# Kernel optimization log

Measured on AMD Instinct MI355X. Metric: run time of the kernel, lower is better.

## Reference

```python
import jax, jax.numpy as jnp
import numpy as np

HIDDEN, FFN, N_EXPERTS, TOP_K = 1024, 2816, 8, 2


def setup_inputs() -> dict:
    key = jax.random.key(0)
    k1, k2, k3, k4, k5 = jax.random.split(key, 5)
    hidden_states = jax.random.normal(k1, (1, 2048, HIDDEN), dtype=jnp.float32)
    # torch Linear weights: [out, in]; experts stacked on leading E axis
    Wgate = jax.random.normal(k2, (N_EXPERTS, HIDDEN), dtype=jnp.float32) * 0.02
    Wg = jax.random.normal(k3, (N_EXPERTS, FFN, HIDDEN), dtype=jnp.float32) * 0.02
    Wu = jax.random.normal(k4, (N_EXPERTS, FFN, HIDDEN), dtype=jnp.float32) * 0.02
    Wd = jax.random.normal(k5, (N_EXPERTS, HIDDEN, FFN), dtype=jnp.float32) * 0.02
    return {"hidden_states": hidden_states, "Wgate": Wgate, "Wg": Wg, "Wu": Wu, "Wd": Wd}


def reference(hidden_states, Wgate, Wg, Wu, Wd):
    x = hidden_states.reshape(-1, hidden_states.shape[-1])  # [T, H]
    # --- router ---
    logits = jnp.einsum('th,eh->te', x, Wgate)               # [T, E]
    weights = jax.nn.softmax(logits, axis=-1)
    topk_w, topk_i = jax.lax.top_k(weights, TOP_K)           # [T, K]
    topk_w = topk_w / jnp.sum(topk_w, axis=-1, keepdims=True)
    # per-token per-expert combine weight (zero if expert not in top-k)
    comb = jnp.sum(jax.nn.one_hot(topk_i, N_EXPERTS, dtype=x.dtype) * topk_w[..., None], axis=1)  # [T, E]
    # --- all-expert SwiGLU (dense reference for the gather-compute-scatter loop) ---
    g = jnp.einsum('th,efh->tef', x, Wg)                     # [T, E, F]
    u = jnp.einsum('th,efh->tef', x, Wu)
    h = jax.nn.silu(g) * u
    y = jnp.einsum('tef,ehf->teh', h, Wd)                    # [T, E, H]
    out = jnp.einsum('te,teh->th', comb, y)                  # [T, H]
    return out
```

## Files before the change

kernel.cpp:

```cpp
#include <hip/hip_runtime.h>
#include <hip/hip_bf16.h>

#define HIDDEN 1024
#define FFN    2816
#define NEXP   8
#define NTOK   2048

typedef __attribute__((ext_vector_type(8))) short short8;
typedef __attribute__((ext_vector_type(4))) short bf16x4;
typedef __attribute__((ext_vector_type(4))) float f32x4;

static __device__ __forceinline__ short f2bf(float f) {
    __hip_bfloat16 h = __float2bfloat16(f);
    return *(short*)&h;
}

static __device__ __forceinline__ void gl_lds16(const short* g, short* l) {
    __builtin_amdgcn_global_load_lds(
        (const __attribute__((address_space(1))) void*)g,
        (__attribute__((address_space(3))) void*)l, 16, 0, 0);
}

#define WAITV(N) asm volatile("s_waitcnt vmcnt(" #N ")" ::: "memory")
#define LGKM0    asm volatile("s_waitcnt lgkmcnt(0)" ::: "memory")
#define BAR()    do { __builtin_amdgcn_s_barrier(); \
                      __builtin_amdgcn_sched_barrier(0); } while (0)

static __device__ __forceinline__ void
router_body(int t, int lane, const float* __restrict__ x,
            const float* __restrict__ Wgate, int* __restrict__ counts,
            int* __restrict__ tok, float* __restrict__ wts)
{
    float acc[NEXP];
#pragma unroll
    for (int e = 0; e < NEXP; e++) acc[e] = 0.f;
    const float* xrow = x + (size_t)t * HIDDEN;
    for (int h = lane; h < HIDDEN; h += 64) {
        float xv = xrow[h];
#pragma unroll
        for (int e = 0; e < NEXP; e++) acc[e] += xv * Wgate[e * HIDDEN + h];
    }
#pragma unroll
    for (int off = 32; off > 0; off >>= 1) {
#pragma unroll
        for (int e = 0; e < NEXP; e++) acc[e] += __shfl_down(acc[e], off);
    }
    if (lane == 0) {
        float mx = acc[0];
#pragma unroll
        for (int e = 1; e < NEXP; e++) mx = fmaxf(mx, acc[e]);
        float p[NEXP];
#pragma unroll
        for (int e = 0; e < NEXP; e++) p[e] = __expf(acc[e] - mx);
        int i0 = 0; float p0 = p[0];
#pragma unroll
        for (int e = 1; e < NEXP; e++) if (p[e] > p0) { p0 = p[e]; i0 = e; }
        int i1 = -1; float p1 = -1.f;
#pragma unroll
        for (int e = 0; e < NEXP; e++) {
            if (e == i0) continue;
            if (p[e] > p1) { p1 = p[e]; i1 = e; }
        }
        float inv = 1.f / (p0 + p1);
        float w0 = p0 * inv, w1 = p1 * inv;
        int s0 = atomicAdd(&counts[i0], 1);
        tok[i0 * NTOK + s0] = t; wts[i0 * NTOK + s0] = w0;
        int s1 = atomicAdd(&counts[i1], 1);
        tok[i1 * NTOK + s1] = t; wts[i1 * NTOK + s1] = w1;
    }
}

__global__ void __launch_bounds__(64)
router_kernel(const float* __restrict__ x, const float* __restrict__ Wgate,
              int* __restrict__ counts, int* __restrict__ tok,
              float* __restrict__ wts)
{
    router_body(blockIdx.x, threadIdx.x, x, Wgate, counts, tok, wts);
}

__global__ void __launch_bounds__(256)
fused_rxz(const float* __restrict__ x, const float* __restrict__ Wgate,
          int* __restrict__ counts, int* __restrict__ tok,
          float* __restrict__ wts, short* __restrict__ xbf,
          float* __restrict__ out)
{
    int bid = blockIdx.x;
    int tid = threadIdx.x;
    if (bid < 512) {
        router_body(bid * 4 + (tid >> 6), tid & 63, x, Wgate, counts, tok, wts);
        return;
    }
    if (bid < 1024) {
        long long base4 = (long long)(bid - 512) * 1024;
#pragma unroll
        for (int p = 0; p < 4; p++) {
            long long r = base4 + p * 256 + tid;
            float4 a = ((const float4*)x)[r];
            bf16x4 o;
            o[0] = f2bf(a.x); o[1] = f2bf(a.y); o[2] = f2bf(a.z); o[3] = f2bf(a.w);
            *(bf16x4*)(xbf + 4 * r) = o;
        }
        return;
    }
    long long base4 = (long long)(bid - 1024) * 1024;
    float4 z = make_float4(0.f, 0.f, 0.f, 0.f);
#pragma unroll
    for (int p = 0; p < 4; p++)
        ((float4*)out)[base4 + p * 256 + tid] = z;
}

#define FFN1_BLOCKS 2816
__global__ void __launch_bounds__(256, 2)
ffn1_v10(const short* __restrict__ xbf, const float* __restrict__ Wg,
         const float* __restrict__ Wu, const int* __restrict__ counts,
         const int* __restrict__ tok, short* __restrict__ hbuf)
{
    int bid = blockIdx.x;
    int tid = threadIdx.x;
    int xb  = bid / 176;
    int yz  = bid - xb * 176;
    int e   = yz / 22;
    int fb  = yz - e * 22;
    int cnt = counts[e];
    int row0 = xb * 128;
    if (row0 >= cnt) return;
    int off_e = 0;
#pragma unroll
    for (int i = 0; i < NEXP; i++) if (i < e) off_e += counts[i];
    int f0 = fb * 128;

    __shared__ short Xs[2][128 * 32];
    __shared__ short Gs[2][128 * 32];
    __shared__ short Us[2][128 * 32];
    __shared__ int   stok[128];

    if (tid < 128) stok[tid] = tok[e * NTOK + min(row0 + tid, cnt - 1)];
    __syncthreads();

    int lane = tid & 63, w = tid >> 6;
    int l15 = lane & 15, lq = lane >> 4;
    int wm = (w & 1) * 64, wn = (w >> 1) * 64;

    int prow   = lane >> 2;
    int gchunk = (lane & 3) ^ ((lane >> 3) & 3);
    const short* xsrc[2]; const float* gsrc[2]; const float* usrc[2];
    int rb[2];
#pragma unroll
    for (int j = 0; j < 2; j++) {
        int rbase = w * 32 + j * 16;
        int r = rbase + prow;
        xsrc[j] = xbf + (size_t)stok[r] * HIDDEN + gchunk * 8;
        gsrc[j] = Wg + (size_t)e * FFN * HIDDEN + (size_t)(f0 + r) * HIDDEN + gchunk * 8;
        usrc[j] = Wu + (size_t)e * FFN * HIDDEN + (size_t)(f0 + r) * HIDDEN + gchunk * 8;
        rb[j] = rbase * 32;
    }
    int wadr0 = rb[0] + lane * 8;
    int wadr1 = rb[1] + lane * 8;

    int aoff[4], boff[4];
#pragma unroll
    for (int mi = 0; mi < 4; mi++) {
        int r = wm + mi * 16 + l15;
        aoff[mi] = r * 32 + (lq ^ ((r >> 1) & 3)) * 8;
    }
#pragma unroll
    for (int ni = 0; ni < 4; ni++) {
        int r = wn + ni * 16 + l15;
        boff[ni] = r * 32 + (lq ^ ((r >> 1) & 3)) * 8;
    }

    f32x4 cg[4][4], cu[4][4];
#pragma unroll
    for (int i = 0; i < 4; i++)
#pragma unroll
        for (int j = 0; j < 4; j++) { cg[i][j] = (f32x4)0.f; cu[i][j] = (f32x4)0.f; }

    float4 g0a, g0b, g1a, g1b, u0a, u0b, u1a, u1b;

#define XDMA(B, T) do { int _k = (T) * 32;                          \
    gl_lds16(xsrc[0] + _k, &Xs[B][rb[0]]);                          \
    gl_lds16(xsrc[1] + _k, &Xs[B][rb[1]]); } while (0)

#define LOADR(T) do { int _k = (T) * 32;                            \
    g0a = *(const float4*)(gsrc[0] + _k);                           \
    g0b = *(const float4*)(gsrc[0] + _k + 4);                       \
    g1a = *(const float4*)(gsrc[1] + _k);                           \
    g1b = *(const float4*)(gsrc[1] + _k + 4);                       \
    u0a = *(const float4*)(usrc[0] + _k);                           \
    u0b = *(const float4*)(usrc[0] + _k + 4);                       \
    u1a = *(const float4*)(usrc[1] + _k);                           \
    u1b = *(const float4*)(usrc[1] + _k + 4); } while (0)

#define PK8(dst, A, Bv) do { short8 _o;                             \
    _o[0] = f2bf(A.x);  _o[1] = f2bf(A.y);                          \
    _o[2] = f2bf(A.z);  _o[3] = f2bf(A.w);                          \
    _o[4] = f2bf(Bv.x); _o[5] = f2bf(Bv.y);                         \
    _o[6] = f2bf(Bv.z); _o[7] = f2bf(Bv.w);                         \
    *(short8*)(dst) = _o; } while (0)

#define CVTW(B) do {                                                \
    PK8(&Gs[B][wadr0], g0a, g0b); PK8(&Gs[B][wadr1], g1a, g1b);     \
    PK8(&Us[B][wadr0], u0a, u0b); PK8(&Us[B][wadr1], u1a, u1b); } while (0)

#define COMP1(B) do {                                               \
    short8 af[4];                                                   \
    _Pragma("unroll")                                               \
    for (int mi = 0; mi < 4; mi++)                                  \
        af[mi] = *(const short8*)&Xs[B][aoff[mi]];                  \
    {   short8 bb[4];                                               \
        _Pragma("unroll")                                           \
        for (int ni = 0; ni < 4; ni++)                              \
            bb[ni] = *(const short8*)&Gs[B][boff[ni]];              \
        _Pragma("unroll")                                           \
        for (int mi = 0; mi < 4; mi++)                              \
        _Pragma("unroll")                                           \
        for (int ni = 0; ni < 4; ni++)                              \
            cg[mi][ni] = __builtin_amdgcn_mfma_f32_16x16x32_bf16(af[mi], bb[ni], cg[mi][ni], 0, 0, 0); \
    }                                                               \
    {   short8 bb[4];                                               \
        _Pragma("unroll")                                           \
        for (int ni = 0; ni < 4; ni++)                              \
            bb[ni] = *(const short8*)&Us[B][boff[ni]];              \
        _Pragma("unroll")                                           \
        for (int mi = 0; mi < 4; mi++)                              \
        _Pragma("unroll")                                           \
        for (int ni = 0; ni < 4; ni++)                              \
            cu[mi][ni] = __builtin_amdgcn_mfma_f32_16x16x32_bf16(af[mi], bb[ni], cu[mi][ni], 0, 0, 0); \
    } } while (0)

    XDMA(0, 0); LOADR(0);

    for (int tt = 0; tt < 32; tt += 2) {
        CVTW(0);
        XDMA(1, tt + 1); LOADR(tt + 1);
        WAITV(10); LGKM0; BAR();
        COMP1(0);
        BAR();
        CVTW(1);
        if (tt + 2 < 32) { XDMA(0, tt + 2); LOADR(tt + 2); WAITV(10); }
        else             { WAITV(0); }
        LGKM0; BAR();
        COMP1(1);
        BAR();
    }

#undef XDMA
#undef LOADR
#undef CVTW
#undef COMP1

#pragma unroll
    for (int mi = 0; mi < 4; mi++)
#pragma unroll
        for (int r = 0; r < 4; r++) {
            int row = wm + mi * 16 + lq * 4 + r;
            int grow = row0 + row;
            if (grow < cnt) {
                short* hrow = hbuf + (size_t)(off_e + grow) * FFN + f0 + wn;
#pragma unroll
                for (int ni = 0; ni < 4; ni++) {
                    float g = cg[mi][ni][r], u = cu[mi][ni][r];
                    float h = g / (1.f + __expf(-g)) * u;
                    hrow[ni * 16 + l15] = f2bf(h);
                }
            }
        }
}

__global__ void __launch_bounds__(256, 2)
ffn2_v9(const short* __restrict__ hbuf, const float* __restrict__ Wd,
        const int* __restrict__ counts, const int* __restrict__ tok,
        const float* __restrict__ wts, float* __restrict__ out)
{
    int bid = blockIdx.x;
    int xb  = bid >> 7;
    int yz  = bid & 127;
    int e   = yz >> 4;
    int y   = yz & 15;
    int cnt = counts[e];
    int row0 = xb * 128;
    if (row0 >= cnt) return;
    int off_e = 0;
#pragma unroll
    for (int i = 0; i < NEXP; i++) if (i < e) off_e += counts[i];
    int h0    = (y >> 1) * 128;
    int kbase = (y & 1) * (FFN / 2);

    __shared__ short Hs[2][128 * 32];
    __shared__ short Ds[2][128 * 32];
    __shared__ int   stok[128];
    __shared__ float swt[128];

    int tid = threadIdx.x;
    if (tid < 128) {
        int rc = min(row0 + tid, cnt - 1);
        stok[tid] = tok[e * NTOK + rc];
        swt[tid]  = wts[e * NTOK + rc];
    }
    __syncthreads();

    int lane = tid & 63, w = tid >> 6;
    int l15 = lane & 15, lq = lane >> 4;
    int wm = (w & 1) * 64, wn = (w >> 1) * 64;

    int prow   = lane >> 2;
    int gchunk = (lane & 3) ^ ((lane >> 3) & 3);
    const short* hsrc[2]; const float* dsrc[2];
    int rb[2];
#pragma unroll
    for (int j = 0; j < 2; j++) {
        int rbase = w * 32 + j * 16;
        int r = rbase + prow;
        hsrc[j] = hbuf + (size_t)(off_e + min(row0 + r, cnt - 1)) * FFN + kbase + gchunk * 8;
        dsrc[j] = Wd + (size_t)e * HIDDEN * FFN + (size_t)(h0 + r) * FFN + kbase + gchunk * 8;
        rb[j] = rbase * 32;
    }
    int wadr0 = rb[0] + lane * 8;
    int wadr1 = rb[1] + lane * 8;

    int aoff[4], boff[4];
#pragma unroll
    for (int mi = 0; mi < 4; mi++) {
        int r = wm + mi * 16 + l15;
        aoff[mi] = r * 32 + (lq ^ ((r >> 1) & 3)) * 8;
    }
#pragma unroll
    for (int ni = 0; ni < 4; ni++) {
        int r = wn + ni * 16 + l15;
        boff[ni] = r * 32 + (lq ^ ((r >> 1) & 3)) * 8;
    }

    f32x4 c[4][4];
#pragma unroll
    for (int i = 0; i < 4; i++)
#pragma unroll
        for (int j = 0; j < 4; j++) c[i][j] = (f32x4)0.f;

    float4 d0a, d0b, d1a, d1b;

#define HDMA(B, T) do { int _k = (T) * 32;                          \
    gl_lds16(hsrc[0] + _k, &Hs[B][rb[0]]);                          \
    gl_lds16(hsrc[1] + _k, &Hs[B][rb[1]]); } while (0)

#define LOADD(T) do { int _k = (T) * 32;                            \
    d0a = *(const float4*)(dsrc[0] + _k);                           \
    d0b = *(const float4*)(dsrc[0] + _k + 4);                       \
    d1a = *(const float4*)(dsrc[1] + _k);                           \
    d1b = *(const float4*)(dsrc[1] + _k + 4); } while (0)

#define CVTD(B) do {                                                \
    PK8(&Ds[B][wadr0], d0a, d0b); PK8(&Ds[B][wadr1], d1a, d1b); } while (0)

#define COMP2(B) do {                                               \
    short8 af[4], bd[4];                                            \
    _Pragma("unroll")                                               \
    for (int mi = 0; mi < 4; mi++)                                  \
        af[mi] = *(const short8*)&Hs[B][aoff[mi]];                  \
    _Pragma("unroll")                                               \
    for (int ni = 0; ni < 4; ni++)                                  \
        bd[ni] = *(const short8*)&Ds[B][boff[ni]];                  \
    _Pragma("unroll")                                               \
    for (int mi = 0; mi < 4; mi++)                                  \
    _Pragma("unroll")                                               \
    for (int ni = 0; ni < 4; ni++)                                  \
        c[mi][ni] = __builtin_amdgcn_mfma_f32_16x16x32_bf16(af[mi], bd[ni], c[mi][ni], 0, 0, 0); \
    } while (0)

    HDMA(0, 0); LOADD(0);

    for (int tt = 0; tt < 44; tt += 2) {
        CVTD(0);
        HDMA(1, tt + 1); LOADD(tt + 1);
        WAITV(6); LGKM0; BAR();
        COMP2(0);
        BAR();
        CVTD(1);
        if (tt + 2 < 44) { HDMA(0, tt + 2); LOADD(tt + 2); WAITV(6); }
        else             { WAITV(0); }
        LGKM0; BAR();
        COMP2(1);
        BAR();
    }

#undef HDMA
#undef LOADD
#undef CVTD
#undef COMP2
#undef PK8

#pragma unroll
    for (int mi = 0; mi < 4; mi++)
#pragma unroll
        for (int r = 0; r < 4; r++) {
            int row = wm + mi * 16 + lq * 4 + r;
            int grow = row0 + row;
            if (grow < cnt) {
                int t = stok[row];
                float wgt = swt[row];
                float* orow = out + (size_t)t * HIDDEN + h0 + wn;
#pragma unroll
                for (int ni = 0; ni < 4; ni++)
                    atomicAdd(&orow[ni * 16 + l15], wgt * c[mi][ni][r]);
            }
        }
}

#define LDW 40
__global__ void __launch_bounds__(256, 2)
ffn1_fb(const float* __restrict__ x, const float* __restrict__ Wg,
        const float* __restrict__ Wu, const int* __restrict__ counts,
        const int* __restrict__ tok, __hip_bfloat16* __restrict__ hbuf)
{
    int e = blockIdx.z;
    int cnt = counts[e];
    int row0 = blockIdx.x * 128;
    if (row0 >= cnt) return;
    int off_e = 0;
#pragma unroll
    for (int i = 0; i < NEXP; i++) if (i < e) off_e += counts[i];
    int f0 = blockIdx.y * 64;

    __shared__ short Xs[128][LDW];
    __shared__ short Gs[64][LDW];
    __shared__ short Us[64][LDW];
    __shared__ int   stok[128];

    int tid = threadIdx.x;
    if (tid < 128) stok[tid] = tok[e * NTOK + min(row0 + tid, cnt - 1)];
    __syncthreads();

    int lane = tid & 63, w = tid >> 6;
    int wm = (w & 1) * 64, wn = (w >> 1) * 32;
    int l15 = lane & 15, lq = lane >> 4;

    f32x4 cg[4][2], cu[4][2];
#pragma unroll
    for (int i = 0; i < 4; i++)
#pragma unroll
        for (int j = 0; j < 2; j++) { cg[i][j] = (f32x4)0.f; cu[i][j] = (f32x4)0.f; }

    const float* Wge = Wg + (size_t)e * FFN * HIDDEN;
    const float* Wue = Wu + (size_t)e * FFN * HIDDEN;

    int xr[4], xc[4]; const float* xp[4];
#pragma unroll
    for (int i = 0; i < 4; i++) {
        int idx = tid + 256 * i;
        xr[i] = idx >> 3; xc[i] = (idx & 7) * 4;
        xp[i] = x + (size_t)stok[xr[i]] * HIDDEN + xc[i];
    }
    int wr[2], wc[2]; const float* gp[2]; const float* up[2];
#pragma unroll
    for (int i = 0; i < 2; i++) {
        int idx = tid + 256 * i;
        wr[i] = idx >> 3; wc[i] = (idx & 7) * 4;
        gp[i] = Wge + (size_t)(f0 + wr[i]) * HIDDEN + wc[i];
        up[i] = Wue + (size_t)(f0 + wr[i]) * HIDDEN + wc[i];
    }

    float4 xa[4], ga[2], ua[2];
#pragma unroll
    for (int i = 0; i < 4; i++) xa[i] = *(const float4*)(xp[i]);
#pragma unroll
    for (int i = 0; i < 2; i++) { ga[i] = *(const float4*)(gp[i]); ua[i] = *(const float4*)(up[i]); }

    for (int k0 = 0; k0 < HIDDEN; k0 += 32) {
        __syncthreads();
#pragma unroll
        for (int i = 0; i < 4; i++) {
            short* d = &Xs[xr[i]][xc[i]];
            d[0] = f2bf(xa[i].x); d[1] = f2bf(xa[i].y);
            d[2] = f2bf(xa[i].z); d[3] = f2bf(xa[i].w);
        }
#pragma unroll
        for (int i = 0; i < 2; i++) {
            short* d = &Gs[wr[i]][wc[i]];
            d[0] = f2bf(ga[i].x); d[1] = f2bf(ga[i].y);
            d[2] = f2bf(ga[i].z); d[3] = f2bf(ga[i].w);
            short* d2 = &Us[wr[i]][wc[i]];
            d2[0] = f2bf(ua[i].x); d2[1] = f2bf(ua[i].y);
            d2[2] = f2bf(ua[i].z); d2[3] = f2bf(ua[i].w);
        }
        __syncthreads();
        if (k0 + 32 < HIDDEN) {
            int kn = k0 + 32;
#pragma unroll
            for (int i = 0; i < 4; i++) xa[i] = *(const float4*)(xp[i] + kn);
#pragma unroll
            for (int i = 0; i < 2; i++) { ga[i] = *(const float4*)(gp[i] + kn); ua[i] = *(const float4*)(up[i] + kn); }
        }
        short8 af[4], bg[2], bu[2];
#pragma unroll
        for (int mi = 0; mi < 4; mi++) af[mi] = *(const short8*)&Xs[wm + mi * 16 + l15][lq * 8];
#pragma unroll
        for (int ni = 0; ni < 2; ni++) {
            bg[ni] = *(const short8*)&Gs[wn + ni * 16 + l15][lq * 8];
            bu[ni] = *(const short8*)&Us[wn + ni * 16 + l15][lq * 8];
        }
#pragma unroll
        for (int mi = 0; mi < 4; mi++)
#pragma unroll
            for (int ni = 0; ni < 2; ni++) {
                cg[mi][ni] = __builtin_amdgcn_mfma_f32_16x16x32_bf16(af[mi], bg[ni], cg[mi][ni], 0, 0, 0);
                cu[mi][ni] = __builtin_amdgcn_mfma_f32_16x16x32_bf16(af[mi], bu[ni], cu[mi][ni], 0, 0, 0);
            }
    }

#pragma unroll
    for (int mi = 0; mi < 4; mi++)
#pragma unroll
        for (int r = 0; r < 4; r++) {
            int row = wm + mi * 16 + lq * 4 + r;
            int grow = row0 + row;
            if (grow < cnt) {
                __hip_bfloat16* hrow = hbuf + (size_t)(off_e + grow) * FFN + f0 + wn;
#pragma unroll
                for (int ni = 0; ni < 2; ni++) {
                    float g = cg[mi][ni][r], u = cu[mi][ni][r];
                    float h = g / (1.f + __expf(-g)) * u;
                    hrow[ni * 16 + l15] = __float2bfloat16(h);
                }
            }
        }
}

__global__ void __launch_bounds__(256, 2)
ffn2_fb(const __hip_bfloat16* __restrict__ hbuf, const float* __restrict__ Wd,
        const int* __restrict__ counts, const int* __restrict__ tok,
        const float* __restrict__ wts, float* __restrict__ out)
{
    int e = blockIdx.z;
    int cnt = counts[e];
    int row0 = blockIdx.x * 128;
    if (row0 >= cnt) return;
    int off_e = 0;
#pragma unroll
    for (int i = 0; i < NEXP; i++) if (i < e) off_e += counts[i];
    int h0 = blockIdx.y * 64;

    __shared__ short Hs[128][LDW];
    __shared__ short Ds[64][LDW];
    __shared__ int   stok[128];
    __shared__ float swt[128];

    int tid = threadIdx.x;
    if (tid < 128) {
        int rc = min(row0 + tid, cnt - 1);
        stok[tid] = tok[e * NTOK + rc];
        swt[tid]  = wts[e * NTOK + rc];
    }
    __syncthreads();

    int lane = tid & 63, w = tid >> 6;
    int wm = (w & 1) * 64, wn = (w >> 1) * 32;
    int l15 = lane & 15, lq = lane >> 4;

    f32x4 c[4][2];
#pragma unroll
    for (int i = 0; i < 4; i++)
#pragma unroll
        for (int j = 0; j < 2; j++) c[i][j] = (f32x4)0.f;

    const float* Wde = Wd + (size_t)e * HIDDEN * FFN;

    int hr[2], hc[2]; const short* hp[2];
#pragma unroll
    for (int i = 0; i < 2; i++) {
        int idx = tid + 256 * i;
        hr[i] = idx >> 2; hc[i] = (idx & 3) * 8;
        int ar = min(row0 + hr[i], cnt - 1);
        hp[i] = (const short*)(hbuf + (size_t)(off_e + ar) * FFN + hc[i]);
    }
    int dr[2], dc[2]; const float* dp[2];
#pragma unroll
    for (int i = 0; i < 2; i++) {
        int idx = tid + 256 * i;
        dr[i] = idx >> 3; dc[i] = (idx & 7) * 4;
        dp[i] = Wde + (size_t)(h0 + dr[i]) * FFN + dc[i];
    }

    short8 ha[2]; float4 da[2];
#pragma unroll
    for (int i = 0; i < 2; i++) { ha[i] = *(const short8*)(hp[i]); da[i] = *(const float4*)(dp[i]); }

    for (int k0 = 0; k0 < FFN; k0 += 32) {
        __syncthreads();
#pragma unroll
        for (int i = 0; i < 2; i++) {
            *(short8*)&Hs[hr[i]][hc[i]] = ha[i];
            short* d = &Ds[dr[i]][dc[i]];
            d[0] = f2bf(da[i].x); d[1] = f2bf(da[i].y);
            d[2] = f2bf(da[i].z); d[3] = f2bf(da[i].w);
        }
        __syncthreads();
        if (k0 + 32 < FFN) {
            int kn = k0 + 32;
#pragma unroll
            for (int i = 0; i < 2; i++) { ha[i] = *(const short8*)(hp[i] + kn); da[i] = *(const float4*)(dp[i] + kn); }
        }
        short8 af[4], bf_[2];
#pragma unroll
        for (int mi = 0; mi < 4; mi++) af[mi] = *(const short8*)&Hs[wm + mi * 16 + l15][lq * 8];
#pragma unroll
        for (int ni = 0; ni < 2; ni++) bf_[ni] = *(const short8*)&Ds[wn + ni * 16 + l15][lq * 8];
#pragma unroll
        for (int mi = 0; mi < 4; mi++)
#pragma unroll
            for (int ni = 0; ni < 2; ni++)
                c[mi][ni] = __builtin_amdgcn_mfma_f32_16x16x32_bf16(af[mi], bf_[ni], c[mi][ni], 0, 0, 0);
    }

#pragma unroll
    for (int mi = 0; mi < 4; mi++)
#pragma unroll
        for (int r = 0; r < 4; r++) {
            int row = wm + mi * 16 + lq * 4 + r;
            int grow = row0 + row;
            if (grow < cnt) {
                int t = stok[row];
                float wgt = swt[row];
                float* orow = out + (size_t)t * HIDDEN + h0 + wn;
#pragma unroll
                for (int ni = 0; ni < 2; ni++)
                    atomicAdd(&orow[ni * 16 + l15], wgt * c[mi][ni][r]);
            }
        }
}

extern "C" void kernel_launch(void* const* d_in, const int* in_sizes, int n_in,
                              void* d_out, int out_size, void* d_ws, size_t ws_size,
                              hipStream_t stream) {
    const float* x     = (const float*)d_in[0];
    const float* Wgate = (const float*)d_in[1];
    const float* Wg    = (const float*)d_in[2];
    const float* Wu    = (const float*)d_in[3];
    const float* Wd    = (const float*)d_in[4];
    float* out = (float*)d_out;

    char* ws = (char*)d_ws;
    int*   counts = (int*)ws;
    int*   tok    = (int*)(ws + 256);
    float* wts    = (float*)(ws + 256 + NEXP * NTOK * 4);

    hipMemsetAsync(counts, 0, 256, stream);

    const size_t base = 256 + 2 * (size_t)NEXP * NTOK * 4;
    const size_t NEED = base
        + 2ull * NTOK * HIDDEN
        + 2ull * 2ull * NTOK * FFN;

    if (ws_size >= NEED) {
        short* xbf  = (short*)(ws + base);
        short* hbuf = xbf + (size_t)NTOK * HIDDEN;

        fused_rxz<<<1536, 256, 0, stream>>>(x, Wgate, counts, tok, wts, xbf, out);

        ffn1_v10<<<FFN1_BLOCKS, 256, 0, stream>>>(xbf, Wg, Wu, counts, tok, hbuf);

        ffn2_v9<<<2048, 256, 0, stream>>>(hbuf, Wd, counts, tok, wts, out);
    } else {
        hipMemsetAsync(out, 0, (size_t)out_size * sizeof(float), stream);
        router_kernel<<<NTOK, 64, 0, stream>>>(x, Wgate, counts, tok, wts);
        __hip_bfloat16* hbuf = (__hip_bfloat16*)(ws + base);
        dim3 g1(NTOK / 128, FFN / 64, NEXP);
        ffn1_fb<<<g1, 256, 0, stream>>>(x, Wg, Wu, counts, tok, hbuf);
        dim3 g2(NTOK / 128, HIDDEN / 64, NEXP);
        ffn2_fb<<<g2, 256, 0, stream>>>(hbuf, Wd, counts, tok, wts, out);
    }
}
```

Baseline: 447.0 us.

## Use 512-thread FFN blocks, read fp32 x directly, fold output zeroing into FFN1

Both FFN kernels move from 256 to 512 threads per block, so each wave owns a 64x32 sub-tile instead of 64x64 and stages one 16-row slice per operand. FFN1 now loads fp32 x rows and converts them to bf16 itself, which removes the separate x-to-bf16 conversion pass and its workspace buffer. Zeroing the output moves into extra blocks of the FFN1 launch, and the router runs as its own small kernel. The cost is that the gathered x rows are read and converted again by every FFN1 block that uses them, and FFN1 loses its async LDS DMA for X in favour of register loads and conversion.

```diff
diff --git a/kernel.cpp b/kernel.cpp
--- a/kernel.cpp
+++ b/kernel.cpp
@@ -13,6 +13,13 @@
 static __device__ __forceinline__ short f2bf(float f) {
     __hip_bfloat16 h = __float2bfloat16(f);
     return *(short*)&h;
+}
+
+static __device__ __forceinline__ void pk8(short* dst, float4 A, float4 B) {
+    short8 o;
+    o[0] = f2bf(A.x); o[1] = f2bf(A.y); o[2] = f2bf(A.z); o[3] = f2bf(A.w);
+    o[4] = f2bf(B.x); o[5] = f2bf(B.y); o[6] = f2bf(B.z); o[7] = f2bf(B.w);
+    *(short8*)dst = o;
 }
 
 static __device__ __forceinline__ void gl_lds16(const short* g, short* l) {
@@ -79,44 +86,31 @@
 }
 
 __global__ void __launch_bounds__(256)
-fused_rxz(const float* __restrict__ x, const float* __restrict__ Wgate,
-          int* __restrict__ counts, int* __restrict__ tok,
-          float* __restrict__ wts, short* __restrict__ xbf,
-          float* __restrict__ out)
+router4(const float* __restrict__ x, const float* __restrict__ Wgate,
+        int* __restrict__ counts, int* __restrict__ tok,
+        float* __restrict__ wts)
+{
+    router_body(blockIdx.x * 4 + (threadIdx.x >> 6), threadIdx.x & 63,
+                x, Wgate, counts, tok, wts);
+}
+
+#define FFN1_BLOCKS 2816
+#define ZERO_BLOCKS 256
+__global__ void __launch_bounds__(512, 2)
+ffn1_v11(const float* __restrict__ x, const float* __restrict__ Wg,
+         const float* __restrict__ Wu, const int* __restrict__ counts,
+         const int* __restrict__ tok, short* __restrict__ hbuf,
+         float* __restrict__ out)
 {
     int bid = blockIdx.x;
     int tid = threadIdx.x;
-    if (bid < 512) {
-        router_body(bid * 4 + (tid >> 6), tid & 63, x, Wgate, counts, tok, wts);
+    if (bid >= FFN1_BLOCKS) {
+        long long b4 = (long long)(bid - FFN1_BLOCKS) * 2048 + tid;
+        float4 z = make_float4(0.f, 0.f, 0.f, 0.f);
+#pragma unroll
+        for (int p = 0; p < 4; p++) ((float4*)out)[b4 + p * 512] = z;
         return;
     }
-    if (bid < 1024) {
-        long long base4 = (long long)(bid - 512) * 1024;
-#pragma unroll
-        for (int p = 0; p < 4; p++) {
-            long long r = base4 + p * 256 + tid;
-            float4 a = ((const float4*)x)[r];
-            bf16x4 o;
-            o[0] = f2bf(a.x); o[1] = f2bf(a.y); o[2] = f2bf(a.z); o[3] = f2bf(a.w);
-            *(bf16x4*)(xbf + 4 * r) = o;
-        }
-        return;
-    }
-    long long base4 = (long long)(bid - 1024) * 1024;
-    float4 z = make_float4(0.f, 0.f, 0.f, 0.f);
-#pragma unroll
-    for (int p = 0; p < 4; p++)
-        ((float4*)out)[base4 + p * 256 + tid] = z;
-}
-
-#define FFN1_BLOCKS 2816
-__global__ void __launch_bounds__(256, 2)
-ffn1_v10(const short* __restrict__ xbf, const float* __restrict__ Wg,
-         const float* __restrict__ Wu, const int* __restrict__ counts,
-         const int* __restrict__ tok, short* __restrict__ hbuf)
-{
-    int bid = blockIdx.x;
-    int tid = threadIdx.x;
     int xb  = bid / 176;
     int yz  = bid - xb * 176;
     int e   = yz / 22;
@@ -132,121 +126,87 @@
     __shared__ short Xs[2][128 * 32];
     __shared__ short Gs[2][128 * 32];
     __shared__ short Us[2][128 * 32];
-    __shared__ int   stok[128];
-
-    if (tid < 128) stok[tid] = tok[e * NTOK + min(row0 + tid, cnt - 1)];
-    __syncthreads();
 
     int lane = tid & 63, w = tid >> 6;
     int l15 = lane & 15, lq = lane >> 4;
-    int wm = (w & 1) * 64, wn = (w >> 1) * 64;
+    int wm = (w & 1) * 64, wn = (w >> 1) * 32;
 
     int prow   = lane >> 2;
     int gchunk = (lane & 3) ^ ((lane >> 3) & 3);
-    const short* xsrc[2]; const float* gsrc[2]; const float* usrc[2];
-    int rb[2];
-#pragma unroll
-    for (int j = 0; j < 2; j++) {
-        int rbase = w * 32 + j * 16;
-        int r = rbase + prow;
-        xsrc[j] = xbf + (size_t)stok[r] * HIDDEN + gchunk * 8;
-        gsrc[j] = Wg + (size_t)e * FFN * HIDDEN + (size_t)(f0 + r) * HIDDEN + gchunk * 8;
-        usrc[j] = Wu + (size_t)e * FFN * HIDDEN + (size_t)(f0 + r) * HIDDEN + gchunk * 8;
-        rb[j] = rbase * 32;
-    }
-    int wadr0 = rb[0] + lane * 8;
-    int wadr1 = rb[1] + lane * 8;
-
-    int aoff[4], boff[4];
+    int rbase  = w * 16;
+    int srow   = min(row0 + rbase + prow, cnt - 1);
+    int tkn    = tok[e * NTOK + srow];
+    const float* xsrc = x  + (size_t)tkn * HIDDEN + gchunk * 8;
+    const float* gsrc = Wg + (size_t)e * FFN * HIDDEN
+                           + (size_t)(f0 + rbase + prow) * HIDDEN + gchunk * 8;
+    const float* usrc = Wu + (size_t)e * FFN * HIDDEN
+                           + (size_t)(f0 + rbase + prow) * HIDDEN + gchunk * 8;
+    int wadr = rbase * 32 + lane * 8;
+
+    int aoff[4], boff[2];
 #pragma unroll
     for (int mi = 0; mi < 4; mi++) {
         int r = wm + mi * 16 + l15;
         aoff[mi] = r * 32 + (lq ^ ((r >> 1) & 3)) * 8;
     }
 #pragma unroll
-    for (int ni = 0; ni < 4; ni++) {
+    for (int ni = 0; ni < 2; ni++) {
         int r = wn + ni * 16 + l15;
         boff[ni] = r * 32 + (lq ^ ((r >> 1) & 3)) * 8;
     }
 
-    f32x4 cg[4][4], cu[4][4];
+    f32x4 cg[4][2], cu[4][2];
 #pragma unroll
     for (int i = 0; i < 4; i++)
 #pragma unroll
-        for (int j = 0; j < 4; j++) { cg[i][j] = (f32x4)0.f; cu[i][j] = (f32x4)0.f; }
-
-    float4 g0a, g0b, g1a, g1b, u0a, u0b, u1a, u1b;
-
-#define XDMA(B, T) do { int _k = (T) * 32;                          \
-    gl_lds16(xsrc[0] + _k, &Xs[B][rb[0]]);                          \
-    gl_lds16(xsrc[1] + _k, &Xs[B][rb[1]]); } while (0)
-
-#define LOADR(T) do { int _k = (T) * 32;                            \
-    g0a = *(const float4*)(gsrc[0] + _k);                           \
-    g0b = *(const float4*)(gsrc[0] + _k + 4);                       \
-    g1a = *(const float4*)(gsrc[1] + _k);                           \
-    g1b = *(const float4*)(gsrc[1] + _k + 4);                       \
-    u0a = *(const float4*)(usrc[0] + _k);                           \
-    u0b = *(const float4*)(usrc[0] + _k + 4);                       \
-    u1a = *(const float4*)(usrc[1] + _k);                           \
-    u1b = *(const float4*)(usrc[1] + _k + 4); } while (0)
-
-#define PK8(dst, A, Bv) do { short8 _o;                             \
-    _o[0] = f2bf(A.x);  _o[1] = f2bf(A.y);                          \
-    _o[2] = f2bf(A.z);  _o[3] = f2bf(A.w);                          \
-    _o[4] = f2bf(Bv.x); _o[5] = f2bf(Bv.y);                         \
-    _o[6] = f2bf(Bv.z); _o[7] = f2bf(Bv.w);                         \
-    *(short8*)(dst) = _o; } while (0)
-
-#define CVTW(B) do {                                                \
-    PK8(&Gs[B][wadr0], g0a, g0b); PK8(&Gs[B][wadr1], g1a, g1b);     \
-    PK8(&Us[B][wadr0], u0a, u0b); PK8(&Us[B][wadr1], u1a, u1b); } while (0)
+        for (int j = 0; j < 2; j++) { cg[i][j] = (f32x4)0.f; cu[i][j] = (f32x4)0.f; }
+
+    float4 xa_, xb_, ga_, gb_, ua_, ub_;
+
+#define LOAD1(T) do { int _k = (T) * 32;                            \
+    xa_ = *(const float4*)(xsrc + _k); xb_ = *(const float4*)(xsrc + _k + 4); \
+    ga_ = *(const float4*)(gsrc + _k); gb_ = *(const float4*)(gsrc + _k + 4); \
+    ua_ = *(const float4*)(usrc + _k); ub_ = *(const float4*)(usrc + _k + 4); } while (0)
+
+#define CVT1(B) do {                                                \
+    pk8(&Xs[B][wadr], xa_, xb_);                                    \
+    pk8(&Gs[B][wadr], ga_, gb_);                                    \
+    pk8(&Us[B][wadr], ua_, ub_); } while (0)
 
 #define COMP1(B) do {                                               \
-    short8 af[4];                                                   \
+    short8 af[4], bg[2], bu[2];                                     \
     _Pragma("unroll")                                               \
     for (int mi = 0; mi < 4; mi++)                                  \
         af[mi] = *(const short8*)&Xs[B][aoff[mi]];                  \
-    {   short8 bb[4];                                               \
-        _Pragma("unroll")                                           \
-        for (int ni = 0; ni < 4; ni++)                              \
-            bb[ni] = *(const short8*)&Gs[B][boff[ni]];              \
-        _Pragma("unroll")                                           \
-        for (int mi = 0; mi < 4; mi++)                              \
-        _Pragma("unroll")                                           \
-        for (int ni = 0; ni < 4; ni++)                              \
-            cg[mi][ni] = __builtin_amdgcn_mfma_f32_16x16x32_bf16(af[mi], bb[ni], cg[mi][ni], 0, 0, 0); \
+    _Pragma("unroll")                                               \
+    for (int ni = 0; ni < 2; ni++) {                                \
+        bg[ni] = *(const short8*)&Gs[B][boff[ni]];                  \
+        bu[ni] = *(const short8*)&Us[B][boff[ni]];                  \
     }                                                               \
-    {   short8 bb[4];                                               \
-        _Pragma("unroll")                                           \
-        for (int ni = 0; ni < 4; ni++)                              \
-            bb[ni] = *(const short8*)&Us[B][boff[ni]];              \
-        _Pragma("unroll")                                           \
-        for (int mi = 0; mi < 4; mi++)                              \
-        _Pragma("unroll")                                           \
-        for (int ni = 0; ni < 4; ni++)                              \
-            cu[mi][ni] = __builtin_amdgcn_mfma_f32_16x16x32_bf16(af[mi], bb[ni], cu[mi][ni], 0, 0, 0); \
+    _Pragma("unroll")                                               \
+    for (int mi = 0; mi < 4; mi++)                                  \
+    _Pragma("unroll")                                               \
+    for (int ni = 0; ni < 2; ni++) {                                \
+        cg[mi][ni] = __builtin_amdgcn_mfma_f32_16x16x32_bf16(af[mi], bg[ni], cg[mi][ni], 0, 0, 0); \
+        cu[mi][ni] = __builtin_amdgcn_mfma_f32_16x16x32_bf16(af[mi], bu[ni], cu[mi][ni], 0, 0, 0); \
     } } while (0)
 
-    XDMA(0, 0); LOADR(0);
-
+    LOAD1(0);
     for (int tt = 0; tt < 32; tt += 2) {
-        CVTW(0);
-        XDMA(1, tt + 1); LOADR(tt + 1);
-        WAITV(10); LGKM0; BAR();
+        CVT1(0);
+        LOAD1(tt + 1);
+        LGKM0; BAR();
         COMP1(0);
         BAR();
-        CVTW(1);
-        if (tt + 2 < 32) { XDMA(0, tt + 2); LOADR(tt + 2); WAITV(10); }
-        else             { WAITV(0); }
+        CVT1(1);
+        if (tt + 2 < 32) LOAD1(tt + 2);
         LGKM0; BAR();
         COMP1(1);
         BAR();
     }
 
-#undef XDMA
-#undef LOADR
-#undef CVTW
+#undef LOAD1
+#undef CVT1
 #undef COMP1
 
 #pragma unroll
@@ -258,7 +218,7 @@
             if (grow < cnt) {
                 short* hrow = hbuf + (size_t)(off_e + grow) * FFN + f0 + wn;
 #pragma unroll
-                for (int ni = 0; ni < 4; ni++) {
+                for (int ni = 0; ni < 2; ni++) {
                     float g = cg[mi][ni][r], u = cu[mi][ni][r];
                     float h = g / (1.f + __expf(-g)) * u;
                     hrow[ni * 16 + l15] = f2bf(h);
@@ -267,10 +227,10 @@
         }
 }
 
-__global__ void __launch_bounds__(256, 2)
-ffn2_v9(const short* __restrict__ hbuf, const float* __restrict__ Wd,
-        const int* __restrict__ counts, const int* __restrict__ tok,
-        const float* __restrict__ wts, float* __restrict__ out)
+__global__ void __launch_bounds__(512, 2)
+ffn2_v11(const short* __restrict__ hbuf, const float* __restrict__ Wd,
+         const int* __restrict__ counts, const int* __restrict__ tok,
+         const float* __restrict__ wts, float* __restrict__ out)
 {
     int bid = blockIdx.x;
     int xb  = bid >> 7;
@@ -301,81 +261,68 @@
 
     int lane = tid & 63, w = tid >> 6;
     int l15 = lane & 15, lq = lane >> 4;
-    int wm = (w & 1) * 64, wn = (w >> 1) * 64;
+    int wm = (w & 1) * 64, wn = (w >> 1) * 32;
 
     int prow   = lane >> 2;
     int gchunk = (lane & 3) ^ ((lane >> 3) & 3);
-    const short* hsrc[2]; const float* dsrc[2];
-    int rb[2];
-#pragma unroll
-    for (int j = 0; j < 2; j++) {
-        int rbase = w * 32 + j * 16;
-        int r = rbase + prow;
-        hsrc[j] = hbuf + (size_t)(off_e + min(row0 + r, cnt - 1)) * FFN + kbase + gchunk * 8;
-        dsrc[j] = Wd + (size_t)e * HIDDEN * FFN + (size_t)(h0 + r) * FFN + kbase + gchunk * 8;
-        rb[j] = rbase * 32;
-    }
-    int wadr0 = rb[0] + lane * 8;
-    int wadr1 = rb[1] + lane * 8;
-
-    int aoff[4], boff[4];
+    int rbase  = w * 16;
+    const short* hsrc = hbuf + (size_t)(off_e + min(row0 + rbase + prow, cnt - 1)) * FFN
+                             + kbase + gchunk * 8;
+    const float* dsrc = Wd + (size_t)e * HIDDEN * FFN
+                           + (size_t)(h0 + rbase + prow) * FFN + kbase + gchunk * 8;
+    int wadr = rbase * 32 + lane * 8;
+
+    int aoff[4], boff[2];
 #pragma unroll
     for (int mi = 0; mi < 4; mi++) {
         int r = wm + mi * 16 + l15;
         aoff[mi] = r * 32 + (lq ^ ((r >> 1) & 3)) * 8;
     }
 #pragma unroll
-    for (int ni = 0; ni < 4; ni++) {
+    for (int ni = 0; ni < 2; ni++) {
         int r = wn + ni * 16 + l15;
         boff[ni] = r * 32 + (lq ^ ((r >> 1) & 3)) * 8;
     }
 
-    f32x4 c[4][4];
+    f32x4 c[4][2];
 #pragma unroll
     for (int i = 0; i < 4; i++)
 #pragma unroll
-        for (int j = 0; j < 4; j++) c[i][j] = (f32x4)0.f;
-
-    float4 d0a, d0b, d1a, d1b;
-
-#define HDMA(B, T) do { int _k = (T) * 32;                          \
-    gl_lds16(hsrc[0] + _k, &Hs[B][rb[0]]);                          \
-    gl_lds16(hsrc[1] + _k, &Hs[B][rb[1]]); } while (0)
+        for (int j = 0; j < 2; j++) c[i][j] = (f32x4)0.f;
+
+    float4 da_, db_;
+
+#define HDMA(B, T) gl_lds16(hsrc + (T) * 32, &Hs[B][rbase * 32])
 
 #define LOADD(T) do { int _k = (T) * 32;                            \
-    d0a = *(const float4*)(dsrc[0] + _k);                           \
-    d0b = *(const float4*)(dsrc[0] + _k + 4);                       \
-    d1a = *(const float4*)(dsrc[1] + _k);                           \
-    d1b = *(const float4*)(dsrc[1] + _k + 4); } while (0)
-
-#define CVTD(B) do {                                                \
-    PK8(&Ds[B][wadr0], d0a, d0b); PK8(&Ds[B][wadr1], d1a, d1b); } while (0)
+    da_ = *(const float4*)(dsrc + _k);                              \
+    db_ = *(const float4*)(dsrc + _k + 4); } while (0)
 
 #define COMP2(B) do {                                               \
-    short8 af[4], bd[4];                                            \
+    short8 af[4], bd[2];                                            \
     _Pragma("unroll")                                               \
     for (int mi = 0; mi < 4; mi++)                                  \
         af[mi] = *(const short8*)&Hs[B][aoff[mi]];                  \
     _Pragma("unroll")                                               \
-    for (int ni = 0; ni < 4; ni++)                                  \
+    for (int ni = 0; ni < 2; ni++)                                  \
         bd[ni] = *(const short8*)&Ds[B][boff[ni]];                  \
     _Pragma("unroll")                                               \
     for (int mi = 0; mi < 4; mi++)                                  \
     _Pragma("unroll")                                               \
-    for (int ni = 0; ni < 4; ni++)                                  \
+    for (int ni = 0; ni < 2; ni++)                                  \
         c[mi][ni] = __builtin_amdgcn_mfma_f32_16x16x32_bf16(af[mi], bd[ni], c[mi][ni], 0, 0, 0); \
     } while (0)
 
     HDMA(0, 0); LOADD(0);
 
     for (int tt = 0; tt < 44; tt += 2) {
-        CVTD(0);
+        pk8(&Ds[0][wadr], da_, db_);
         HDMA(1, tt + 1); LOADD(tt + 1);
-        WAITV(6); LGKM0; BAR();
+        WAITV(3); LGKM0; BAR();
         COMP2(0);
         BAR();
-        CVTD(1);
-        if (tt + 2 < 44) { HDMA(0, tt + 2); LOADD(tt + 2); WAITV(6); }
+        pk8(&Ds[1][wadr], da_, db_);
+        if (tt + 2 < 44) { HDMA(0, tt + 2); LOADD(tt + 2); WAITV(3); }
         else             { WAITV(0); }
         LGKM0; BAR();
         COMP2(1);
@@ -384,9 +331,7 @@
 
 #undef HDMA
 #undef LOADD
-#undef CVTD
 #undef COMP2
-#undef PK8
 
 #pragma unroll
     for (int mi = 0; mi < 4; mi++)
@@ -399,7 +344,7 @@
                 float wgt = swt[row];
                 float* orow = out + (size_t)t * HIDDEN + h0 + wn;
 #pragma unroll
-                for (int ni = 0; ni < 4; ni++)
+                for (int ni = 0; ni < 2; ni++)
                     atomicAdd(&orow[ni * 16 + l15], wgt * c[mi][ni][r]);
             }
         }
@@ -645,19 +590,17 @@
     hipMemsetAsync(counts, 0, 256, stream);
 
     const size_t base = 256 + 2 * (size_t)NEXP * NTOK * 4;
-    const size_t NEED = base
-        + 2ull * NTOK * HIDDEN
-        + 2ull * 2ull * NTOK * FFN;
+    const size_t NEED = base + 2ull * 2ull * NTOK * FFN;
 
     if (ws_size >= NEED) {
-        short* xbf  = (short*)(ws + base);
-        short* hbuf = xbf + (size_t)NTOK * HIDDEN;
-
-        fused_rxz<<<1536, 256, 0, stream>>>(x, Wgate, counts, tok, wts, xbf, out);
-
-        ffn1_v10<<<FFN1_BLOCKS, 256, 0, stream>>>(xbf, Wg, Wu, counts, tok, hbuf);
-
-        ffn2_v9<<<2048, 256, 0, stream>>>(hbuf, Wd, counts, tok, wts, out);
+        short* hbuf = (short*)(ws + base);
+
+        router4<<<512, 256, 0, stream>>>(x, Wgate, counts, tok, wts);
+
+        ffn1_v11<<<FFN1_BLOCKS + ZERO_BLOCKS, 512, 0, stream>>>(
+            x, Wg, Wu, counts, tok, hbuf, out);
+
+        ffn2_v11<<<2048, 512, 0, stream>>>(hbuf, Wd, counts, tok, wts, out);
     } else {
         hipMemsetAsync(out, 0, (size_t)out_size * sizeof(float), stream);
         router_kernel<<<NTOK, 64, 0, stream>>>(x, Wgate, counts, tok, wts);
```

Result: slower. 482.0 us (+7.8%).

## Double token tile to 256 rows with 512-thread blocks in both FFN kernels

Applied to the files above, without the earlier changes.

Both expert GEMM kernels now process 256 gathered tokens per block using eight waves instead of 128 tokens with four waves. Each wave loads one 16-row slice of the fp32 weight tile rather than two, and the launch grids are halved. The goal is to halve how many times each expert's fp32 weights are read from memory and converted to bf16, since that weight traffic dominates. The costs are more LDS per block, higher register pressure at 512 threads, and more wasted padded rows for experts whose token count is not a multiple of 256.

```diff
diff --git a/kernel.cpp b/kernel.cpp
--- a/kernel.cpp
+++ b/kernel.cpp
@@ -13,6 +13,13 @@
 static __device__ __forceinline__ short f2bf(float f) {
     __hip_bfloat16 h = __float2bfloat16(f);
     return *(short*)&h;
+}
+
+static __device__ __forceinline__ void pk8(short* dst, float4 A, float4 B) {
+    short8 o;
+    o[0] = f2bf(A.x); o[1] = f2bf(A.y); o[2] = f2bf(A.z); o[3] = f2bf(A.w);
+    o[4] = f2bf(B.x); o[5] = f2bf(B.y); o[6] = f2bf(B.z); o[7] = f2bf(B.w);
+    *(short8*)dst = o;
 }
 
 static __device__ __forceinline__ void gl_lds16(const short* g, short* l) {
@@ -109,9 +116,9 @@
         ((float4*)out)[base4 + p * 256 + tid] = z;
 }
 
-#define FFN1_BLOCKS 2816
-__global__ void __launch_bounds__(256, 2)
-ffn1_v10(const short* __restrict__ xbf, const float* __restrict__ Wg,
+#define FFN1_BLOCKS 1408
+__global__ void __launch_bounds__(512, 2)
+ffn1_v12(const short* __restrict__ xbf, const float* __restrict__ Wg,
          const float* __restrict__ Wu, const int* __restrict__ counts,
          const int* __restrict__ tok, short* __restrict__ hbuf)
 {
@@ -122,40 +129,40 @@
     int e   = yz / 22;
     int fb  = yz - e * 22;
     int cnt = counts[e];
-    int row0 = xb * 128;
+    int row0 = xb * 256;
     if (row0 >= cnt) return;
     int off_e = 0;
 #pragma unroll
     for (int i = 0; i < NEXP; i++) if (i < e) off_e += counts[i];
     int f0 = fb * 128;
 
-    __shared__ short Xs[2][128 * 32];
+    __shared__ short Xs[2][256 * 32];
     __shared__ short Gs[2][128 * 32];
     __shared__ short Us[2][128 * 32];
-    __shared__ int   stok[128];
-
-    if (tid < 128) stok[tid] = tok[e * NTOK + min(row0 + tid, cnt - 1)];
+    __shared__ int   stok[256];
+
+    if (tid < 256) stok[tid] = tok[e * NTOK + min(row0 + tid, cnt - 1)];
     __syncthreads();
 
     int lane = tid & 63, w = tid >> 6;
     int l15 = lane & 15, lq = lane >> 4;
-    int wm = (w & 1) * 64, wn = (w >> 1) * 64;
+    int wm = (w & 3) * 64, wn = (w >> 2) * 64;
 
     int prow   = lane >> 2;
     int gchunk = (lane & 3) ^ ((lane >> 3) & 3);
-    const short* xsrc[2]; const float* gsrc[2]; const float* usrc[2];
-    int rb[2];
+
+    const short* xsrc[2]; int xrb[2];
 #pragma unroll
     for (int j = 0; j < 2; j++) {
         int rbase = w * 32 + j * 16;
-        int r = rbase + prow;
-        xsrc[j] = xbf + (size_t)stok[r] * HIDDEN + gchunk * 8;
-        gsrc[j] = Wg + (size_t)e * FFN * HIDDEN + (size_t)(f0 + r) * HIDDEN + gchunk * 8;
-        usrc[j] = Wu + (size_t)e * FFN * HIDDEN + (size_t)(f0 + r) * HIDDEN + gchunk * 8;
-        rb[j] = rbase * 32;
-    }
-    int wadr0 = rb[0] + lane * 8;
-    int wadr1 = rb[1] + lane * 8;
+        xsrc[j] = xbf + (size_t)stok[rbase + prow] * HIDDEN + gchunk * 8;
+        xrb[j] = rbase * 32;
+    }
+    const float* gsrc = Wg + (size_t)e * FFN * HIDDEN
+                           + (size_t)(f0 + w * 16 + prow) * HIDDEN + gchunk * 8;
+    const float* usrc = Wu + (size_t)e * FFN * HIDDEN
+                           + (size_t)(f0 + w * 16 + prow) * HIDDEN + gchunk * 8;
+    int wadr = (w * 16) * 32 + lane * 8;
 
     int aoff[4], boff[4];
 #pragma unroll
@@ -175,32 +182,19 @@
 #pragma unroll
         for (int j = 0; j < 4; j++) { cg[i][j] = (f32x4)0.f; cu[i][j] = (f32x4)0.f; }
 
-    float4 g0a, g0b, g1a, g1b, u0a, u0b, u1a, u1b;
+    float4 ga_, gb_, ua_, ub_;
 
 #define XDMA(B, T) do { int _k = (T) * 32;                          \
-    gl_lds16(xsrc[0] + _k, &Xs[B][rb[0]]);                          \
-    gl_lds16(xsrc[1] + _k, &Xs[B][rb[1]]); } while (0)
+    gl_lds16(xsrc[0] + _k, &Xs[B][xrb[0]]);                         \
+    gl_lds16(xsrc[1] + _k, &Xs[B][xrb[1]]); } while (0)
 
 #define LOADR(T) do { int _k = (T) * 32;                            \
-    g0a = *(const float4*)(gsrc[0] + _k);                           \
-    g0b = *(const float4*)(gsrc[0] + _k + 4);                       \
-    g1a = *(const float4*)(gsrc[1] + _k);                           \
-    g1b = *(const float4*)(gsrc[1] + _k + 4);                       \
-    u0a = *(const float4*)(usrc[0] + _k);                           \
-    u0b = *(const float4*)(usrc[0] + _k + 4);                       \
-    u1a = *(const float4*)(usrc[1] + _k);                           \
-    u1b = *(const float4*)(usrc[1] + _k + 4); } while (0)
-
-#define PK8(dst, A, Bv) do { short8 _o;                             \
-    _o[0] = f2bf(A.x);  _o[1] = f2bf(A.y);                          \
-    _o[2] = f2bf(A.z);  _o[3] = f2bf(A.w);                          \
-    _o[4] = f2bf(Bv.x); _o[5] = f2bf(Bv.y);                         \
-    _o[6] = f2bf(Bv.z); _o[7] = f2bf(Bv.w);                         \
-    *(short8*)(dst) = _o; } while (0)
+    ga_ = *(const float4*)(gsrc + _k); gb_ = *(const float4*)(gsrc + _k + 4); \
+    ua_ = *(const float4*)(usrc + _k); ub_ = *(const float4*)(usrc + _k + 4); } while (0)
 
 #define CVTW(B) do {                                                \
-    PK8(&Gs[B][wadr0], g0a, g0b); PK8(&Gs[B][wadr1], g1a, g1b);     \
-    PK8(&Us[B][wadr0], u0a, u0b); PK8(&Us[B][wadr1], u1a, u1b); } while (0)
+    pk8(&Gs[B][wadr], ga_, gb_);                                    \
+    pk8(&Us[B][wadr], ua_, ub_); } while (0)
 
 #define COMP1(B) do {                                               \
     short8 af[4];                                                   \
@@ -233,11 +227,11 @@
     for (int tt = 0; tt < 32; tt += 2) {
         CVTW(0);
         XDMA(1, tt + 1); LOADR(tt + 1);
-        WAITV(10); LGKM0; BAR();
+        WAITV(6); LGKM0; BAR();
         COMP1(0);
         BAR();
         CVTW(1);
-        if (tt + 2 < 32) { XDMA(0, tt + 2); LOADR(tt + 2); WAITV(10); }
+        if (tt + 2 < 32) { XDMA(0, tt + 2); LOADR(tt + 2); WAITV(6); }
         else             { WAITV(0); }
         LGKM0; BAR();
         COMP1(1);
@@ -267,10 +261,10 @@
         }
 }
 
-__global__ void __launch_bounds__(256, 2)
-ffn2_v9(const short* __restrict__ hbuf, const float* __restrict__ Wd,
-        const int* __restrict__ counts, const int* __restrict__ tok,
-        const float* __restrict__ wts, float* __restrict__ out)
+__global__ void __launch_bounds__(512, 2)
+ffn2_v12(const short* __restrict__ hbuf, const float* __restrict__ Wd,
+         const int* __restrict__ counts, const int* __restrict__ tok,
+         const float* __restrict__ wts, float* __restrict__ out)
 {
     int bid = blockIdx.x;
     int xb  = bid >> 7;
@@ -278,7 +272,7 @@
     int e   = yz >> 4;
     int y   = yz & 15;
     int cnt = counts[e];
-    int row0 = xb * 128;
+    int row0 = xb * 256;
     if (row0 >= cnt) return;
     int off_e = 0;
 #pragma unroll
@@ -286,13 +280,13 @@
     int h0    = (y >> 1) * 128;
     int kbase = (y & 1) * (FFN / 2);
 
-    __shared__ short Hs[2][128 * 32];
+    __shared__ short Hs[2][256 * 32];
     __shared__ short Ds[2][128 * 32];
-    __shared__ int   stok[128];
-    __shared__ float swt[128];
+    __shared__ int   stok[256];
+    __shared__ float swt[256];
 
     int tid = threadIdx.x;
-    if (tid < 128) {
+    if (tid < 256) {
         int rc = min(row0 + tid, cnt - 1);
         stok[tid] = tok[e * NTOK + rc];
         swt[tid]  = wts[e * NTOK + rc];
@@ -301,22 +295,22 @@
 
     int lane = tid & 63, w = tid >> 6;
     int l15 = lane & 15, lq = lane >> 4;
-    int wm = (w & 1) * 64, wn = (w >> 1) * 64;
+    int wm = (w & 3) * 64, wn = (w >> 2) * 64;
 
     int prow   = lane >> 2;
     int gchunk = (lane & 3) ^ ((lane >> 3) & 3);
-    const short* hsrc[2]; const float* dsrc[2];
-    int rb[2];
+
+    const short* hsrc[2]; int hrb[2];
 #pragma unroll
     for (int j = 0; j < 2; j++) {
         int rbase = w * 32 + j * 16;
-        int r = rbase + prow;
-        hsrc[j] = hbuf + (size_t)(off_e + min(row0 + r, cnt - 1)) * FFN + kbase + gchunk * 8;
-        dsrc[j] = Wd + (size_t)e * HIDDEN * FFN + (size_t)(h0 + r) * FFN + kbase + gchunk * 8;
-        rb[j] = rbase * 32;
-    }
-    int wadr0 = rb[0] + lane * 8;
-    int wadr1 = rb[1] + lane * 8;
+        hsrc[j] = hbuf + (size_t)(off_e + min(row0 + rbase + prow, cnt - 1)) * FFN
+                       + kbase + gchunk * 8;
+        hrb[j] = rbase * 32;
+    }
+    const float* dsrc = Wd + (size_t)e * HIDDEN * FFN
+                           + (size_t)(h0 + w * 16 + prow) * FFN + kbase + gchunk * 8;
+    int wadr = (w * 16) * 32 + lane * 8;
 
     int aoff[4], boff[4];
 #pragma unroll
@@ -336,20 +330,15 @@
 #pragma unroll
         for (int j = 0; j < 4; j++) c[i][j] = (f32x4)0.f;
 
-    float4 d0a, d0b, d1a, d1b;
+    float4 da_, db_;
 
 #define HDMA(B, T) do { int _k = (T) * 32;                          \
-    gl_lds16(hsrc[0] + _k, &Hs[B][rb[0]]);                          \
-    gl_lds16(hsrc[1] + _k, &Hs[B][rb[1]]); } while (0)
+    gl_lds16(hsrc[0] + _k, &Hs[B][hrb[0]]);                         \
+    gl_lds16(hsrc[1] + _k, &Hs[B][hrb[1]]); } while (0)
 
 #define LOADD(T) do { int _k = (T) * 32;                            \
-    d0a = *(const float4*)(dsrc[0] + _k);                           \
-    d0b = *(const float4*)(dsrc[0] + _k + 4);                       \
-    d1a = *(const float4*)(dsrc[1] + _k);                           \
-    d1b = *(const float4*)(dsrc[1] + _k + 4); } while (0)
-
-#define CVTD(B) do {                                                \
-    PK8(&Ds[B][wadr0], d0a, d0b); PK8(&Ds[B][wadr1], d1a, d1b); } while (0)
+    da_ = *(const float4*)(dsrc + _k);                              \
+    db_ = *(const float4*)(dsrc + _k + 4); } while (0)
 
 #define COMP2(B) do {                                               \
     short8 af[4], bd[4];                                            \
@@ -369,13 +358,13 @@
     HDMA(0, 0); LOADD(0);
 
     for (int tt = 0; tt < 44; tt += 2) {
-        CVTD(0);
+        pk8(&Ds[0][wadr], da_, db_);
         HDMA(1, tt + 1); LOADD(tt + 1);
-        WAITV(6); LGKM0; BAR();
+        WAITV(4); LGKM0; BAR();
         COMP2(0);
         BAR();
-        CVTD(1);
-        if (tt + 2 < 44) { HDMA(0, tt + 2); LOADD(tt + 2); WAITV(6); }
+        pk8(&Ds[1][wadr], da_, db_);
+        if (tt + 2 < 44) { HDMA(0, tt + 2); LOADD(tt + 2); WAITV(4); }
         else             { WAITV(0); }
         LGKM0; BAR();
         COMP2(1);
@@ -384,9 +373,7 @@
 
 #undef HDMA
 #undef LOADD
-#undef CVTD
 #undef COMP2
-#undef PK8
 
 #pragma unroll
     for (int mi = 0; mi < 4; mi++)
@@ -655,9 +642,9 @@
 
         fused_rxz<<<1536, 256, 0, stream>>>(x, Wgate, counts, tok, wts, xbf, out);
 
-        ffn1_v10<<<FFN1_BLOCKS, 256, 0, stream>>>(xbf, Wg, Wu, counts, tok, hbuf);
-
-        ffn2_v9<<<2048, 256, 0, stream>>>(hbuf, Wd, counts, tok, wts, out);
+        ffn1_v12<<<FFN1_BLOCKS, 512, 0, stream>>>(xbf, Wg, Wu, counts, tok, hbuf);
+
+        ffn2_v12<<<1024, 512, 0, stream>>>(hbuf, Wd, counts, tok, wts, out);
     } else {
         hipMemsetAsync(out, 0, (size_t)out_size * sizeof(float), stream);
         router_kernel<<<NTOK, 64, 0, stream>>>(x, Wgate, counts, tok, wts);
```

After: 448.6 us. No clear change (+0.3%).
